# Kernel optimization log

Hardware: AMD Instinct MI355X
Metric: run time of the kernel (lower is better)

The kernel has to match this reference:

```python
import jax, jax.numpy as jnp
import numpy as np

PAD = 2  # kernel_height // 2 for kernel_height=5


def earth_pad2d(x, ph, pw):
    # circular pad in longitude (last dim), zero pad in latitude (dim 2)
    if pw > 0:
        x = jnp.concatenate([x[..., -pw:], x, x[..., :pw]], axis=-1)
    if ph > 0:
        x = jnp.pad(x, ((0, 0), (0, 0), (ph, ph), (0, 0)))
    return x


def earth_wrap2d(x, w, pad):
    # fold circular overhang of a transposed-conv output back onto width w
    core = x[..., pad:pad + w]
    rw = x.shape[-1] - pad - w  # right overhang (stride-1... here 1)
    core = core.at[..., :rw].add(x[..., pad + w:])
    core = core.at[..., w - pad:].add(x[..., :pad])
    return core


def _conv(x, w, b, stride):
    # torch Conv2d, weight [Cout, Cin, 1, k], VALID padding, stride (1, stride)
    y = jax.lax.conv_general_dilated(x, w, (1, stride), 'VALID',
                                     dimension_numbers=('NCHW', 'OIHW', 'NCHW'))
    return y + b[None, :, None, None]


def _convT(x, w, stride):
    # torch ConvTranspose2d (no bias), weight [Cin, Cout, 1, k], padding 0
    k = w.shape[-1]
    wr = jnp.transpose(jnp.flip(w, axis=(2, 3)), (1, 0, 2, 3))  # -> [Cout, Cin, 1, k]
    return jax.lax.conv_general_dilated(x, wr, (1, 1),
                                        [(0, 0), (k - 1, k - 1)],
                                        lhs_dilation=(1, stride),
                                        dimension_numbers=('NCHW', 'OIHW', 'NCHW'))


def _edge(x, d, p):
    return x[:, :, -p:, :] if d == 1 else x[:, :, :p, :]


def _set_edge(x, d, p, v):
    return x.at[:, :, -p:, :].set(v) if d == 1 else x.at[:, :, :p, :].set(v)


def _forward(strips, wi, wo):
    strips_pad = [earth_pad2d(s, PAD, PAD) for s in strips]
    # center strip inner edges from the adjacent coarser strips (to_inners[0])
    for d in (-1, 1):
        a = _edge(strips[2 + d], -d, PAD)
        a = _convT(a, wi[0], 2)
        a = earth_wrap2d(a, strips[2].shape[3], 2)
        a = earth_pad2d(a, 0, PAD)
        strips_pad[2] = _set_edge(strips_pad[2], d, PAD, a)
    # outer strips: far edge from next coarser (to_inners), near edge from finer (to_outers)
    for mi in (1, 2):
        for d in (-1, 1):
            idx = 2 + d * mi
            sp = strips_pad[idx]
            if mi + 1 <= 2:
                o = _edge(strips[2 + d * (mi + 1)], -d, PAD)
                o = _convT(o, wi[mi], 2)
                o = earth_wrap2d(o, strips[idx].shape[3], 2)
                o = earth_pad2d(o, 0, PAD)
                sp = _set_edge(sp, d, PAD, o)
            en = _edge(strips[2 + d * (mi - 1)], d, PAD)
            en = earth_pad2d(en, 0, 2)
            en = _conv(en, wo[mi - 1][0], wo[mi - 1][1], 2)
            en = earth_pad2d(en, 0, PAD)
            sp = _set_edge(sp, -d, PAD, en)
            strips_pad[idx] = sp
    return tuple(strips_pad)


def setup_inputs():
    key = jax.random.key(0)
    ks = jax.random.split(key, 11)
    B, C, W = 1, 256, 1440
    shapes = [(B, C, 30, W // 4), (B, C, 60, W // 2), (B, C, 180, W),
              (B, C, 60, W // 2), (B, C, 30, W // 4)]
    d = {}
    for i, sh in enumerate(shapes):
        d['s%d' % i] = jax.random.normal(ks[i], sh, dtype=jnp.float32)
    scale = 0.03
    d['wi0'] = jax.random.normal(ks[5], (C, C, 1, 5), dtype=jnp.float32) * scale
    d['wi1'] = jax.random.normal(ks[6], (C, C, 1, 5), dtype=jnp.float32) * scale
    d['wo0'] = jax.random.normal(ks[7], (C, C, 1, 5), dtype=jnp.float32) * scale
    d['bo0'] = jax.random.normal(ks[8], (C,), dtype=jnp.float32) * 0.01
    d['wo1'] = jax.random.normal(ks[9], (C, C, 1, 5), dtype=jnp.float32) * scale
    d['bo1'] = jax.random.normal(ks[10], (C,), dtype=jnp.float32) * 0.01
    return d


def reference(s0, s1, s2, s3, s4, wi0, wi1, wo0, bo0, wo1, bo1):
    return _forward([s0, s1, s2, s3, s4], [wi0, wi1], [(wo0, bo0), (wo1, bo1)])
```

## Files before the change

### kernel.cpp

```cpp
#include <hip/hip_runtime.h>


struct ConvJob {
  const float* x; const float* wt; const float* bias; float* out;
  int Hin, Win, r0, Hout, Wcore, h0, type, bpr;
};
struct ConvJobs { ConvJob j[8]; };

__global__ __launch_bounds__(256) void transpose_w_kernel(const float* __restrict__ src,
                                                          float* __restrict__ dst, int mode) {
  int idx = blockIdx.x * 256 + threadIdx.x;
  int oc = idx & 255;
  int t = idx >> 8;
  int k = t % 5;
  int ic = t / 5;
  float v = (mode == 0) ? src[(ic * 256 + oc) * 5 + k] : src[(oc * 256 + ic) * 5 + k];
  dst[idx] = v;
}

__global__ __launch_bounds__(256) void pad_copy_kernel(const float* __restrict__ in,
                                                       float* __restrict__ out, int H, int W) {
  int WO4 = (W >> 2) + 1;
  int id = blockIdx.x * 256 + threadIdx.x;
  int w4 = id % WO4;
  int hz = id / WO4;
  int h = hz % H;
  int c = hz / H;
  const float* src = in + ((size_t)(c * H + h)) * W;
  int wc = w4 * 4;
  float4 v;
  if (w4 >= 1 && wc <= W - 4) {
    float2 a = *(const float2*)(src + wc - 2);
    float2 b = *(const float2*)(src + wc);
    v = make_float4(a.x, a.y, b.x, b.y);
  } else {
    int c0 = wc - 2 + W;
    v.x = src[c0 % W];
    v.y = src[(c0 + 1) % W];
    v.z = src[(c0 + 2) % W];
    v.w = src[(c0 + 3) % W];
  }
  *(float4*)(out + ((size_t)(c * (H + 4) + h + 2)) * (W + 4) + wc) = v;
}

__global__ __launch_bounds__(256) void zero_rows_kernel(float* __restrict__ out,
                                                        int Hout, int Wout, int h0) {
  int id = blockIdx.x * 256 + threadIdx.x;
  if (id >= 256 * 2 * Wout) return;
  int w = id % Wout;
  int t = id / Wout;
  int r = t & 1;
  int c = t >> 1;
  out[((size_t)(c * Hout + h0 + r)) * Wout + w] = 0.f;
}

__global__ __launch_bounds__(256) void conv_all_kernel(ConvJobs js) {
  const ConvJob jb = js.j[blockIdx.y];
  int bx = blockIdx.x;
  if (bx >= 2 * jb.bpr) return;
  int tile = bx >> 1;
  int r = bx & 1;
  int t = threadIdx.x;
  __shared__ float xs[19 * 256];
  const int Win = jb.Win;
  const float* xrow = jb.x + ((size_t)(t * jb.Hin + jb.r0 + r)) * Win;
  const float* wt = jb.wt + t;
  const int Wop = jb.Wcore + 4;
  float* orow = jb.out + ((size_t)(t * jb.Hout + jb.h0 + r)) * Wop;

  if (jb.type == 1) {
    int u0 = tile * 8;
    int cb = 2 * u0 - 2;
#pragma unroll
    for (int cc = 0; cc < 19; ++cc) {
      int col = cb + cc;
      col += (col < 0) ? Win : 0;
      col -= (col >= Win) ? Win : 0;
      xs[cc * 256 + t] = xrow[col];
    }
    __syncthreads();
    float acc[8];
    float bv = jb.bias[t];
#pragma unroll
    for (int i = 0; i < 8; ++i) acc[i] = bv;
    for (int ic0 = 0; ic0 < 256; ic0 += 4) {
      float4 xv[19];
#pragma unroll
      for (int cc = 0; cc < 19; ++cc) xv[cc] = *(const float4*)&xs[cc * 256 + ic0];
      float w[4][5];
#pragma unroll
      for (int i = 0; i < 4; ++i)
#pragma unroll
        for (int k = 0; k < 5; ++k) w[i][k] = wt[((ic0 + i) * 5 + k) * 256];
#pragma unroll
      for (int u = 0; u < 8; ++u)
#pragma unroll
        for (int k = 0; k < 5; ++k) {
          float4 xq = xv[2 * u + k];
          acc[u] += w[0][k] * xq.x + w[1][k] * xq.y + w[2][k] * xq.z + w[3][k] * xq.w;
        }
    }
#pragma unroll
    for (int i = 0; i < 8; ++i) {
      int g = u0 + i;
      float vv = acc[i];
      orow[2 + g] = vv;
      if (g < 2) orow[jb.Wcore + 2 + g] = vv;
      if (g >= jb.Wcore - 2) orow[g - (jb.Wcore - 2)] = vv;
    }
  } else {
    int m0 = tile * 16;
    int jb0 = (m0 >> 1) - 1;
#pragma unroll
    for (int cc = 0; cc < 10; ++cc) {
      int col = jb0 + cc;
      col += (col < 0) ? Win : 0;
      col -= (col >= Win) ? Win : 0;
      xs[cc * 256 + t] = xrow[col];
    }
    __syncthreads();
    float acc[16];
#pragma unroll
    for (int i = 0; i < 16; ++i) acc[i] = 0.f;
    for (int ic0 = 0; ic0 < 256; ic0 += 4) {
      float4 xv[10];
#pragma unroll
      for (int cc = 0; cc < 10; ++cc) xv[cc] = *(const float4*)&xs[cc * 256 + ic0];
      float w[4][5];
#pragma unroll
      for (int i = 0; i < 4; ++i)
#pragma unroll
        for (int k = 0; k < 5; ++k) w[i][k] = wt[((ic0 + i) * 5 + k) * 256];
#pragma unroll
      for (int ml = 0; ml < 16; ++ml) {
        if ((ml & 1) == 0) {
#pragma unroll
          for (int kk = 0; kk < 3; ++kk) {
            int k = 2 * kk;
            float4 xq = xv[(ml + 4 - k) >> 1];
            acc[ml] += w[0][k] * xq.x + w[1][k] * xq.y + w[2][k] * xq.z + w[3][k] * xq.w;
          }
        } else {
#pragma unroll
          for (int kk = 0; kk < 2; ++kk) {
            int k = 2 * kk + 1;
            float4 xq = xv[(ml + 4 - k) >> 1];
            acc[ml] += w[0][k] * xq.x + w[1][k] * xq.y + w[2][k] * xq.z + w[3][k] * xq.w;
          }
        }
      }
    }
#pragma unroll
    for (int i = 0; i < 16; ++i) {
      int g = m0 + i;
      float vv = acc[i];
      orow[2 + g] = vv;
      if (g < 2) orow[jb.Wcore + 2 + g] = vv;
      if (g >= jb.Wcore - 2) orow[g - (jb.Wcore - 2)] = vv;
    }
  }
}

extern "C" void kernel_launch(void* const* d_in, const int* in_sizes, int n_in,
                              void* d_out, int out_size, void* d_ws, size_t ws_size,
                              hipStream_t stream) {
  const float* s0 = (const float*)d_in[0];
  const float* s1 = (const float*)d_in[1];
  const float* s2 = (const float*)d_in[2];
  const float* s3 = (const float*)d_in[3];
  const float* s4 = (const float*)d_in[4];
  const float* wi0 = (const float*)d_in[5];
  const float* wi1 = (const float*)d_in[6];
  const float* wo0 = (const float*)d_in[7];
  const float* bo0 = (const float*)d_in[8];
  const float* wo1 = (const float*)d_in[9];
  const float* bo1 = (const float*)d_in[10];

  float* out = (float*)d_out;
  float* out0 = out;
  float* out1 = out + 3168256;
  float* out2 = out + 15030272;
  float* out3 = out + 83048448;
  float* out4 = out + 94910464;

  float* wt0 = (float*)d_ws;
  float* wt1 = wt0 + 327680;
  float* wt2 = wt1 + 327680;
  float* wt3 = wt2 + 327680;
  transpose_w_kernel<<<1280, 256, 0, stream>>>(wi0, wt0, 0);
  transpose_w_kernel<<<1280, 256, 0, stream>>>(wi1, wt1, 0);
  transpose_w_kernel<<<1280, 256, 0, stream>>>(wo0, wt2, 1);
  transpose_w_kernel<<<1280, 256, 0, stream>>>(wo1, wt3, 1);

  ConvJobs js;
  js.j[0] = {s1, wt0, nullptr, out2,  60,  720,  58, 184, 1440,   0, 0, 90};
  js.j[1] = {s3, wt0, nullptr, out2,  60,  720,   0, 184, 1440, 182, 0, 90};
  js.j[2] = {s0, wt1, nullptr, out1,  30,  360,  28,  64,  720,   0, 0, 45};
  js.j[3] = {s4, wt1, nullptr, out3,  30,  360,   0,  64,  720,  62, 0, 45};
  js.j[4] = {s2, wt2, bo0,     out1, 180, 1440,   0,  64,  720,  62, 1, 90};
  js.j[5] = {s2, wt2, bo0,     out3, 180, 1440, 178,  64,  720,   0, 1, 90};
  js.j[6] = {s1, wt3, bo1,     out0,  60,  720,   0,  34,  360,  32, 1, 45};
  js.j[7] = {s3, wt3, bo1,     out4,  60,  720,  58,  34,  360,   0, 1, 45};
  conv_all_kernel<<<dim3(180, 8), 256, 0, stream>>>(js);

  pad_copy_kernel<<<30 * 91, 256, 0, stream>>>(s0, out0, 30, 360);
  pad_copy_kernel<<<60 * 181, 256, 0, stream>>>(s1, out1, 60, 720);
  pad_copy_kernel<<<180 * 361, 256, 0, stream>>>(s2, out2, 180, 1440);
  pad_copy_kernel<<<60 * 181, 256, 0, stream>>>(s3, out3, 60, 720);
  pad_copy_kernel<<<30 * 91, 256, 0, stream>>>(s4, out4, 30, 360);

  zero_rows_kernel<<<(256 * 2 * 364 + 255) / 256, 256, 0, stream>>>(out0, 34, 364, 0);
  zero_rows_kernel<<<(256 * 2 * 364 + 255) / 256, 256, 0, stream>>>(out4, 34, 364, 32);
}
```

Measured before the change: 338.2 us.

## Fuse conv, pad-copy and zero-row kernels into one mega kernel launch

Merges the four weight-transpose launches into one, and folds the 8-job conv, five pad-copy launches and two zero-row launches into a single block-indexed mega kernel. The conv job grid is flattened with per-job block offsets, so the idle blocks of the old 2D grid go away. The inner loops now stream xs columns from LDS one at a time instead of holding all 19 or 10 float4s in registers, which aims to cut register pressure. The cost is that the conv blocks and the many cheap copy blocks share one launch, and its 19×256 static LDS allocation applies to every block.

```diff
diff --git a/kernel.cpp b/kernel.cpp
--- a/kernel.cpp
+++ b/kernel.cpp
@@ -3,25 +3,34 @@
 
 struct ConvJob {
   const float* x; const float* wt; const float* bias; float* out;
-  int Hin, Win, r0, Hout, Wcore, h0, type, bpr;
+  int Hin, Win, r0, Hout, Wcore, h0, type, blk_start;
 };
-struct ConvJobs { ConvJob j[8]; };
-
-__global__ __launch_bounds__(256) void transpose_w_kernel(const float* __restrict__ src,
-                                                          float* __restrict__ dst, int mode) {
-  int idx = blockIdx.x * 256 + threadIdx.x;
+
+struct MegaParams {
+  ConvJob j[8];
+  const float* in0; const float* in1; const float* in2; const float* in3; const float* in4;
+  float* o0; float* o1; float* o2; float* o3; float* o4;
+};
+
+struct WTParams { const float* src[4]; float* dst[4]; };
+
+__global__ __launch_bounds__(256) void transpose_all_kernel(WTParams p) {
+  int b = blockIdx.x;
+  int which = b / 1280;
+  int idx = (b - which * 1280) * 256 + threadIdx.x;
   int oc = idx & 255;
-  int t = idx >> 8;
-  int k = t % 5;
-  int ic = t / 5;
-  float v = (mode == 0) ? src[(ic * 256 + oc) * 5 + k] : src[(oc * 256 + ic) * 5 + k];
-  dst[idx] = v;
-}
-
-__global__ __launch_bounds__(256) void pad_copy_kernel(const float* __restrict__ in,
-                                                       float* __restrict__ out, int H, int W) {
-  int WO4 = (W >> 2) + 1;
-  int id = blockIdx.x * 256 + threadIdx.x;
+  int q = idx >> 8;
+  int k = q % 5;
+  int ic = q / 5;
+  const float* s = p.src[which];
+  float v = (which < 2) ? s[(ic * 256 + oc) * 5 + k] : s[(oc * 256 + ic) * 5 + k];
+  p.dst[which][idx] = v;
+}
+
+template <int H, int W>
+__device__ __forceinline__ void copy_strip(const float* __restrict__ in,
+                                           float* __restrict__ out, int id) {
+  constexpr int WO4 = W / 4 + 1;
   int w4 = id % WO4;
   int hz = id / WO4;
   int h = hz % H;
@@ -43,25 +52,9 @@
   *(float4*)(out + ((size_t)(c * (H + 4) + h + 2)) * (W + 4) + wc) = v;
 }
 
-__global__ __launch_bounds__(256) void zero_rows_kernel(float* __restrict__ out,
-                                                        int Hout, int Wout, int h0) {
-  int id = blockIdx.x * 256 + threadIdx.x;
-  if (id >= 256 * 2 * Wout) return;
-  int w = id % Wout;
-  int t = id / Wout;
-  int r = t & 1;
-  int c = t >> 1;
-  out[((size_t)(c * Hout + h0 + r)) * Wout + w] = 0.f;
-}
-
-__global__ __launch_bounds__(256) void conv_all_kernel(ConvJobs js) {
-  const ConvJob jb = js.j[blockIdx.y];
-  int bx = blockIdx.x;
-  if (bx >= 2 * jb.bpr) return;
-  int tile = bx >> 1;
-  int r = bx & 1;
-  int t = threadIdx.x;
-  __shared__ float xs[19 * 256];
+__device__ __forceinline__ void conv_block(const ConvJob jb, int local, int t, float* xs) {
+  int tile = local >> 1;
+  int r = local & 1;
   const int Win = jb.Win;
   const float* xrow = jb.x + ((size_t)(t * jb.Hin + jb.r0 + r)) * Win;
   const float* wt = jb.wt + t;
@@ -79,26 +72,26 @@
       xs[cc * 256 + t] = xrow[col];
     }
     __syncthreads();
+    float bv = jb.bias[t];
     float acc[8];
-    float bv = jb.bias[t];
 #pragma unroll
     for (int i = 0; i < 8; ++i) acc[i] = bv;
     for (int ic0 = 0; ic0 < 256; ic0 += 4) {
-      float4 xv[19];
-#pragma unroll
-      for (int cc = 0; cc < 19; ++cc) xv[cc] = *(const float4*)&xs[cc * 256 + ic0];
       float w[4][5];
 #pragma unroll
       for (int i = 0; i < 4; ++i)
 #pragma unroll
         for (int k = 0; k < 5; ++k) w[i][k] = wt[((ic0 + i) * 5 + k) * 256];
 #pragma unroll
-      for (int u = 0; u < 8; ++u)
-#pragma unroll
-        for (int k = 0; k < 5; ++k) {
-          float4 xq = xv[2 * u + k];
-          acc[u] += w[0][k] * xq.x + w[1][k] * xq.y + w[2][k] * xq.z + w[3][k] * xq.w;
+      for (int cc = 0; cc < 19; ++cc) {
+        float4 xq = *(const float4*)&xs[cc * 256 + ic0];
+#pragma unroll
+        for (int i = 0; i < 8; ++i) {
+          int k = cc - 2 * i;
+          if (k >= 0 && k < 5)
+            acc[i] += w[0][k] * xq.x + w[1][k] * xq.y + w[2][k] * xq.z + w[3][k] * xq.w;
         }
+      }
     }
 #pragma unroll
     for (int i = 0; i < 8; ++i) {
@@ -110,10 +103,10 @@
     }
   } else {
     int m0 = tile * 16;
-    int jb0 = (m0 >> 1) - 1;
+    int j0 = (m0 >> 1) - 1;
 #pragma unroll
     for (int cc = 0; cc < 10; ++cc) {
-      int col = jb0 + cc;
+      int col = j0 + cc;
       col += (col < 0) ? Win : 0;
       col -= (col >= Win) ? Win : 0;
       xs[cc * 256 + t] = xrow[col];
@@ -123,30 +116,19 @@
 #pragma unroll
     for (int i = 0; i < 16; ++i) acc[i] = 0.f;
     for (int ic0 = 0; ic0 < 256; ic0 += 4) {
-      float4 xv[10];
-#pragma unroll
-      for (int cc = 0; cc < 10; ++cc) xv[cc] = *(const float4*)&xs[cc * 256 + ic0];
       float w[4][5];
 #pragma unroll
       for (int i = 0; i < 4; ++i)
 #pragma unroll
         for (int k = 0; k < 5; ++k) w[i][k] = wt[((ic0 + i) * 5 + k) * 256];
 #pragma unroll
-      for (int ml = 0; ml < 16; ++ml) {
-        if ((ml & 1) == 0) {
-#pragma unroll
-          for (int kk = 0; kk < 3; ++kk) {
-            int k = 2 * kk;
-            float4 xq = xv[(ml + 4 - k) >> 1];
+      for (int cc = 0; cc < 10; ++cc) {
+        float4 xq = *(const float4*)&xs[cc * 256 + ic0];
+#pragma unroll
+        for (int ml = 0; ml < 16; ++ml) {
+          int k = ml + 4 - 2 * cc;
+          if (k >= 0 && k < 5)
             acc[ml] += w[0][k] * xq.x + w[1][k] * xq.y + w[2][k] * xq.z + w[3][k] * xq.w;
-          }
-        } else {
-#pragma unroll
-          for (int kk = 0; kk < 2; ++kk) {
-            int k = 2 * kk + 1;
-            float4 xq = xv[(ml + 4 - k) >> 1];
-            acc[ml] += w[0][k] * xq.x + w[1][k] * xq.y + w[2][k] * xq.z + w[3][k] * xq.w;
-          }
         }
       }
     }
@@ -158,6 +140,40 @@
       if (g < 2) orow[jb.Wcore + 2 + g] = vv;
       if (g >= jb.Wcore - 2) orow[g - (jb.Wcore - 2)] = vv;
     }
+  }
+}
+
+__global__ __launch_bounds__(256) void mega_kernel(MegaParams p) {
+  __shared__ float xs[19 * 256];
+  int bx = blockIdx.x;
+  int t = threadIdx.x;
+  if (bx < 1080) {
+    int ji = 0;
+#pragma unroll
+    for (int i = 1; i < 8; ++i)
+      if (bx >= p.j[i].blk_start) ji = i;
+    conv_block(p.j[ji], bx - p.j[ji].blk_start, t, xs);
+  } else if (bx < 3810) {
+    copy_strip<30, 360>(p.in0, p.o0, (bx - 1080) * 256 + t);
+  } else if (bx < 14670) {
+    copy_strip<60, 720>(p.in1, p.o1, (bx - 3810) * 256 + t);
+  } else if (bx < 79650) {
+    copy_strip<180, 1440>(p.in2, p.o2, (bx - 14670) * 256 + t);
+  } else if (bx < 90510) {
+    copy_strip<60, 720>(p.in3, p.o3, (bx - 79650) * 256 + t);
+  } else if (bx < 93240) {
+    copy_strip<30, 360>(p.in4, p.o4, (bx - 90510) * 256 + t);
+  } else {
+    int id = (bx - 93240) * 256 + t;
+    int w4 = id % 91;
+    int t2 = id / 91;
+    int strip = t2 >> 9;
+    int cr = t2 & 511;
+    int c = cr >> 1;
+    int r = cr & 1;
+    float* o = (strip == 0) ? p.o0 + ((size_t)(c * 34 + r)) * 364
+                            : p.o4 + ((size_t)(c * 34 + 32 + r)) * 364;
+    *(float4*)(o + w4 * 4) = make_float4(0.f, 0.f, 0.f, 0.f);
   }
 }
 
@@ -187,28 +203,23 @@
   float* wt1 = wt0 + 327680;
   float* wt2 = wt1 + 327680;
   float* wt3 = wt2 + 327680;
-  transpose_w_kernel<<<1280, 256, 0, stream>>>(wi0, wt0, 0);
-  transpose_w_kernel<<<1280, 256, 0, stream>>>(wi1, wt1, 0);
-  transpose_w_kernel<<<1280, 256, 0, stream>>>(wo0, wt2, 1);
-  transpose_w_kernel<<<1280, 256, 0, stream>>>(wo1, wt3, 1);
-
-  ConvJobs js;
-  js.j[0] = {s1, wt0, nullptr, out2,  60,  720,  58, 184, 1440,   0, 0, 90};
-  js.j[1] = {s3, wt0, nullptr, out2,  60,  720,   0, 184, 1440, 182, 0, 90};
-  js.j[2] = {s0, wt1, nullptr, out1,  30,  360,  28,  64,  720,   0, 0, 45};
-  js.j[3] = {s4, wt1, nullptr, out3,  30,  360,   0,  64,  720,  62, 0, 45};
-  js.j[4] = {s2, wt2, bo0,     out1, 180, 1440,   0,  64,  720,  62, 1, 90};
-  js.j[5] = {s2, wt2, bo0,     out3, 180, 1440, 178,  64,  720,   0, 1, 90};
-  js.j[6] = {s1, wt3, bo1,     out0,  60,  720,   0,  34,  360,  32, 1, 45};
-  js.j[7] = {s3, wt3, bo1,     out4,  60,  720,  58,  34,  360,   0, 1, 45};
-  conv_all_kernel<<<dim3(180, 8), 256, 0, stream>>>(js);
-
-  pad_copy_kernel<<<30 * 91, 256, 0, stream>>>(s0, out0, 30, 360);
-  pad_copy_kernel<<<60 * 181, 256, 0, stream>>>(s1, out1, 60, 720);
-  pad_copy_kernel<<<180 * 361, 256, 0, stream>>>(s2, out2, 180, 1440);
-  pad_copy_kernel<<<60 * 181, 256, 0, stream>>>(s3, out3, 60, 720);
-  pad_copy_kernel<<<30 * 91, 256, 0, stream>>>(s4, out4, 30, 360);
-
-  zero_rows_kernel<<<(256 * 2 * 364 + 255) / 256, 256, 0, stream>>>(out0, 34, 364, 0);
-  zero_rows_kernel<<<(256 * 2 * 364 + 255) / 256, 256, 0, stream>>>(out4, 34, 364, 32);
-}
+
+  WTParams wp;
+  wp.src[0] = wi0; wp.src[1] = wi1; wp.src[2] = wo0; wp.src[3] = wo1;
+  wp.dst[0] = wt0; wp.dst[1] = wt1; wp.dst[2] = wt2; wp.dst[3] = wt3;
+  transpose_all_kernel<<<5120, 256, 0, stream>>>(wp);
+
+  MegaParams mp;
+  mp.j[0] = {s1, wt0, nullptr, out2,  60,  720,  58, 184, 1440,   0, 0,   0};
+  mp.j[1] = {s3, wt0, nullptr, out2,  60,  720,   0, 184, 1440, 182, 0, 180};
+  mp.j[2] = {s0, wt1, nullptr, out1,  30,  360,  28,  64,  720,   0, 0, 360};
+  mp.j[3] = {s4, wt1, nullptr, out3,  30,  360,   0,  64,  720,  62, 0, 450};
+  mp.j[4] = {s2, wt2, bo0,     out1, 180, 1440,   0,  64,  720,  62, 1, 540};
+  mp.j[5] = {s2, wt2, bo0,     out3, 180, 1440, 178,  64,  720,   0, 1, 720};
+  mp.j[6] = {s1, wt3, bo1,     out0,  60,  720,   0,  34,  360,  32, 1, 900};
+  mp.j[7] = {s3, wt3, bo1,     out4,  60,  720,  58,  34,  360,   0, 1, 990};
+  mp.in0 = s0; mp.in1 = s1; mp.in2 = s2; mp.in3 = s3; mp.in4 = s4;
+  mp.o0 = out0; mp.o1 = out1; mp.o2 = out2; mp.o3 = out3; mp.o4 = out4;
+
+  mega_kernel<<<93604, 256, 0, stream>>>(mp);
+}
```

Measured after the change: 348.5 us. 1.03x slower.
